# Kernel optimization log

Measured on AMD Instinct MI355X. Metric: run time of the kernel, lower is better.

Reference implementation:

```python
import jax, jax.numpy as jnp
import numpy as np

N, E = 10000, 100000
WIDTH, KER_WIDTH, DEPTH = 32, 128, 3
EDGE_ATTR_DIM, IN_WIDTH, OUT_WIDTH, COORD_DIM = 6, 3, 1, 3


def _glorot(k, fan_in, fan_out):
    return jax.random.normal(k, (fan_in, fan_out), jnp.float32) / np.sqrt(fan_in).astype(np.float32)


def setup_inputs() -> dict:
    key = jax.random.key(0)
    ks = jax.random.split(key, 16)
    z = lambda n: jnp.zeros((n,), jnp.float32)
    return {
        "x": jax.random.normal(ks[0], (N, IN_WIDTH), jnp.float32),
        "edge_index": jax.random.randint(ks[1], (2, E), 0, N),
        "edge_attr": jax.random.normal(ks[2], (E, EDGE_ATTR_DIM), jnp.float32),
        "coords_init": jax.random.normal(ks[3], (N, COORD_DIM), jnp.float32),
        "fc1_w": _glorot(ks[4], IN_WIDTH, WIDTH), "fc1_b": z(WIDTH),
        "ker_w1": _glorot(ks[5], EDGE_ATTR_DIM + 1, KER_WIDTH // 2), "ker_b1": z(KER_WIDTH // 2),
        "ker_w2": _glorot(ks[6], KER_WIDTH // 2, KER_WIDTH), "ker_b2": z(KER_WIDTH),
        "ker_w3": _glorot(ks[7], KER_WIDTH, WIDTH * WIDTH), "ker_b3": z(WIDTH * WIDTH),
        "cm_w1": _glorot(ks[8], WIDTH, WIDTH), "cm_b1": z(WIDTH),
        "cm_w2": _glorot(ks[9], WIDTH, 1) * 1e-3,  # xavier gain=0.001 coord head, no bias
        "fc2_w1": _glorot(ks[10], WIDTH, 2 * WIDTH), "fc2_b1": z(2 * WIDTH),
        "fc2_w2": _glorot(ks[11], 2 * WIDTH, OUT_WIDTH), "fc2_b2": z(OUT_WIDTH),
    }


def _seg_mean(data, seg, n):
    s = jax.ops.segment_sum(data, seg, num_segments=n)
    c = jax.ops.segment_sum(jnp.ones((seg.shape[0], 1), data.dtype), seg, num_segments=n)
    return s / jnp.clip(c, 1.0)


def reference(x, edge_index, edge_attr, coords_init,
              fc1_w, fc1_b, ker_w1, ker_b1, ker_w2, ker_b2, ker_w3, ker_b3,
              cm_w1, cm_b1, cm_w2, fc2_w1, fc2_b1, fc2_w2, fc2_b2):
    row, col = edge_index[0], edge_index[1]
    h = x @ fc1_w + fc1_b                                   # [N, W]
    coord = coords_init
    for _ in range(DEPTH):
        coord_diff = coord[row] - coord[col]                # [E, 3]
        radial = jnp.sum(coord_diff * coord_diff, axis=-1, keepdims=True)
        kin = jnp.concatenate([edge_attr, radial], axis=-1)  # [E, ker_in]
        k = jax.nn.relu(kin @ ker_w1 + ker_b1)
        k = jax.nn.relu(k @ ker_w2 + ker_b2)
        Wk = (k @ ker_w3 + ker_b3).reshape(E, WIDTH, WIDTH)  # per-edge kernel matrix
        m = jnp.einsum('eij,ej->ei', Wk, h[col])             # per-edge message [E, W]
        phi = jax.nn.relu(m @ cm_w1 + cm_b1) @ cm_w2         # [E, 1]
        coord = coord + _seg_mean(coord_diff * phi, row, N)  # equivariant coord update
        h = jax.nn.relu(h + _seg_mean(m, row, N))            # GKN node update
    out = jax.nn.relu(h @ fc2_w1 + fc2_b1) @ fc2_w2 + fc2_b2  # [N, out_width]
    return out, coord
```

## Files before the change

### kernel.cpp

```cpp
#include <hip/hip_runtime.h>
#include <hip/hip_bf16.h>

#define NN 10000
#define NE 100000

typedef __bf16 bf16x8 __attribute__((ext_vector_type(8)));
typedef float  f32x4  __attribute__((ext_vector_type(4)));

__device__ __forceinline__ f32x4 relu4(f32x4 a) {
    a.x = fmaxf(a.x, 0.f); a.y = fmaxf(a.y, 0.f);
    a.z = fmaxf(a.z, 0.f); a.w = fmaxf(a.w, 0.f);
    return a;
}


__global__ void k_deg(const int* __restrict__ eidx, int* __restrict__ deg) {
    int e = blockIdx.x * blockDim.x + threadIdx.x;
    if (e < NE) atomicAdd(&deg[eidx[e]], 1);
}

__global__ void k_scan(const int* __restrict__ deg, int* __restrict__ rowptr,
                       int* __restrict__ cursor, float* __restrict__ deg_inv) {
    __shared__ int ssum[256];
    const int tid = threadIdx.x;
    const int CH = 40;
    const int base = tid * CH;
    int s = 0;
    for (int i = 0; i < CH; ++i) { int n = base + i; if (n < NN) s += deg[n]; }
    ssum[tid] = s;
    __syncthreads();
    for (int off = 1; off < 256; off <<= 1) {
        int t = (tid >= off) ? ssum[tid - off] : 0;
        __syncthreads();
        ssum[tid] += t;
        __syncthreads();
    }
    int run = ssum[tid] - s;
    for (int i = 0; i < CH; ++i) {
        int n = base + i;
        if (n < NN) {
            int d = deg[n];
            rowptr[n] = run; cursor[n] = run; run += d;
            deg_inv[n] = 1.0f / (float)(d > 1 ? d : 1);
        }
    }
    if (tid == 255) rowptr[NN] = ssum[255];
}

__global__ void k_fill(const int* __restrict__ eidx, int* __restrict__ cursor,
                       int* __restrict__ ebyrow, int* __restrict__ pos_r) {
    int e = blockIdx.x * blockDim.x + threadIdx.x;
    if (e < NE) {
        int r = eidx[e];
        int slot = atomicAdd(&cursor[r], 1);
        ebyrow[slot] = e;
        pos_r[e] = slot;
    }
}

__global__ void k_setup(const float* __restrict__ w3, __bf16* __restrict__ w3sw,
                        const float* __restrict__ w2, __bf16* __restrict__ w2sw,
                        const float* __restrict__ x, const float* __restrict__ fc1w,
                        const float* __restrict__ fc1b, const float* __restrict__ cinit,
                        float* __restrict__ h, float* __restrict__ coord) {
    int t = blockIdx.x * blockDim.x + threadIdx.x;
    if (t < 131072) {
        int jj = t & 7;
        int L  = (t >> 3) & 63;
        int ks = (t >> 9) & 3;
        int jt = (t >> 11) & 1;
        int i  = t >> 12;
        int c    = ks*32 + (L >> 4)*8 + jj;
        int colv = i*32 + jt*16 + (L & 15);
        w3sw[t] = (__bf16)w3[c*1024 + colv];
    } else if (t < 139264) {
        int u = t - 131072;
        int jj = u & 7;
        int L  = (u >> 3) & 63;
        int ks = (u >> 9) & 1;
        int nt = u >> 10;
        int c1 = ks*32 + (L >> 4)*8 + jj;
        int c2 = nt*16 + (L & 15);
        w2sw[u] = (__bf16)w2[c1*128 + c2];
    } else if (t < 139264 + NN) {
        int n = t - 139264;
        float x0 = x[n*3+0], x1 = x[n*3+1], x2 = x[n*3+2];
        #pragma unroll
        for (int j = 0; j < 32; j += 4) {
            f32x4 a = *(const f32x4*)(fc1b + j);
            a += x0 * (*(const f32x4*)(fc1w + 0*32 + j));
            a += x1 * (*(const f32x4*)(fc1w + 1*32 + j));
            a += x2 * (*(const f32x4*)(fc1w + 2*32 + j));
            *(f32x4*)(h + n*32 + j) = a;
        }
        coord[n*3+0] = cinit[n*3+0];
        coord[n*3+1] = cinit[n*3+1];
        coord[n*3+2] = cinit[n*3+2];
    }
}

__global__ __launch_bounds__(256, 2)
void k_layer(const float* __restrict__ coord, const int* __restrict__ eidx,
             const float* __restrict__ eattr,
             const float* __restrict__ w1, const float* __restrict__ b1,
             const __bf16* __restrict__ w2sw, const float* __restrict__ b2,
             const __bf16* __restrict__ w3sw, const float* __restrict__ b3,
             const float* __restrict__ h,
             const float* __restrict__ cm_w1, const float* __restrict__ cm_b1,
             const float* __restrict__ cm_w2, const int* __restrict__ pos_r,
             float* __restrict__ cds, float* __restrict__ m_s,
             float* __restrict__ phis) {
    __shared__ float smem[4 * 64 * 36];
    __bf16* kt1 = (__bf16*)smem;
    __bf16* kt2 = (__bf16*)smem + 4608;
    const int lane = threadIdx.x & 63;
    const int wave = threadIdx.x >> 6;
    const int q = lane >> 4, t = lane & 15;
    const int base = blockIdx.x * 64;

    const int eg = base + lane;
    const int egc = eg < NE ? eg : NE - 1;
    const bool wvalid = eg < NE;
    const int pos = pos_r[egc];

    int col = eidx[NE + egc];
    float hcol[32];
    {
        const f32x4* hp = (const f32x4*)(h + (size_t)col * 32);
        #pragma unroll
        for (int v = 0; v < 8; ++v) {
            f32x4 hv = hp[v];
            hcol[v*4+0] = hv.x; hcol[v*4+1] = hv.y; hcol[v*4+2] = hv.z; hcol[v*4+3] = hv.w;
        }
    }
    bf16x8 bcur[8];
    {
        const __bf16* wb0 = w3sw + (size_t)(wave * 8) * 4096;
        #pragma unroll
        for (int f = 0; f < 8; ++f)
            bcur[f] = *(const bf16x8*)(wb0 + (f*64 + lane) * 8);
    }

    {
        int r = eidx[egc];
        float dx = coord[r*3+0] - coord[col*3+0];
        float dy = coord[r*3+1] - coord[col*3+1];
        float dz = coord[r*3+2] - coord[col*3+2];
        float rad = dx*dx + dy*dy + dz*dz;
        if (wave == 0 && wvalid) {
            f32x4 cdv = {dx, dy, dz, rad};
            *(f32x4*)(cds + (size_t)pos*4) = cdv;
        }
        float kin[7];
        #pragma unroll
        for (int a = 0; a < 6; ++a) kin[a] = eattr[(size_t)egc*6 + a];
        kin[6] = rad;

        const int g0 = wave * 16;
        f32x4 acc1[4];
        #pragma unroll
        for (int g = 0; g < 4; ++g) acc1[g] = *(const f32x4*)(b1 + g0 + g*4);
        #pragma unroll
        for (int t7 = 0; t7 < 7; ++t7) {
            float kv = kin[t7];
            #pragma unroll
            for (int g = 0; g < 4; ++g)
                acc1[g] += kv * (*(const f32x4*)(w1 + t7*64 + g0 + g*4));
        }
        #pragma unroll
        for (int cc = 0; cc < 2; ++cc) {
            f32x4 a0 = relu4(acc1[cc*2]), a1 = relu4(acc1[cc*2+1]);
            bf16x8 pk = {(__bf16)a0.x, (__bf16)a0.y, (__bf16)a0.z, (__bf16)a0.w,
                         (__bf16)a1.x, (__bf16)a1.y, (__bf16)a1.z, (__bf16)a1.w};
            int chunk = wave*2 + cc;
            *(bf16x8*)(kt1 + lane*72 + ((chunk ^ (lane & 7)) * 8)) = pk;
        }
    }
    __syncthreads();

    {
        bf16x8 af[4][2];
        #pragma unroll
        for (int mt = 0; mt < 4; ++mt) {
            int ep = mt*16 + t;
            #pragma unroll
            for (int ks = 0; ks < 2; ++ks)
                af[mt][ks] = *(const bf16x8*)(kt1 + ep*72 + (((ks*4 + q) ^ (ep & 7)) * 8));
        }
        #pragma unroll
        for (int nn = 0; nn < 2; ++nn) {
            int nt = wave*2 + nn;
            f32x4 a2[4];
            #pragma unroll
            for (int mt = 0; mt < 4; ++mt) a2[mt] = (f32x4){0.f, 0.f, 0.f, 0.f};
            #pragma unroll
            for (int ks = 0; ks < 2; ++ks) {
                bf16x8 bf_ = *(const bf16x8*)(w2sw + ((nt*2 + ks)*64 + lane) * 8);
                #pragma unroll
                for (int mt = 0; mt < 4; ++mt)
                    a2[mt] = __builtin_amdgcn_mfma_f32_16x16x32_bf16(af[mt][ks], bf_, a2[mt], 0, 0, 0);
            }
            float bias = b2[nt*16 + t];
            int chunk = nt*2 + (t >> 3);
            int tin = t & 7;
            #pragma unroll
            for (int mt = 0; mt < 4; ++mt) {
                #pragma unroll
                for (int rr = 0; rr < 4; ++rr) {
                    int row = mt*16 + q*4 + rr;
                    kt2[row*128 + ((chunk ^ (row & 15)) * 8) + tin] =
                        (__bf16)fmaxf(a2[mt][rr] + bias, 0.f);
                }
            }
        }
    }
    __syncthreads();

    bf16x8 afrag[4][4];
    #pragma unroll
    for (int mt = 0; mt < 4; ++mt) {
        int ep = mt*16 + t;
        #pragma unroll
        for (int ks = 0; ks < 4; ++ks) {
            int ck = ks*4 + q;
            afrag[mt][ks] = *(const bf16x8*)(kt2 + ep*128 + ((ck ^ (ep & 15)) * 8));
        }
    }
    __syncthreads();

    float* wkw = smem + wave * (64 * 36);
    const float* wkrow = wkw + lane * 36;
    float mv[8];

    #pragma unroll
    for (int ii = 0; ii < 8; ++ii) {
        const int i = wave * 8 + ii;
        f32x4 acc[4][2];
        #pragma unroll
        for (int mt = 0; mt < 4; ++mt) {
            acc[mt][0] = (f32x4){0.f, 0.f, 0.f, 0.f};
            acc[mt][1] = (f32x4){0.f, 0.f, 0.f, 0.f};
        }
        #pragma unroll
        for (int jt = 0; jt < 2; ++jt) {
            #pragma unroll
            for (int ks = 0; ks < 4; ++ks) {
                bf16x8 bfrag = bcur[jt*4 + ks];
                #pragma unroll
                for (int mt = 0; mt < 4; ++mt)
                    acc[mt][jt] = __builtin_amdgcn_mfma_f32_16x16x32_bf16(
                        afrag[mt][ks], bfrag, acc[mt][jt], 0, 0, 0);
            }
        }
        if (ii < 7) {
            const __bf16* wbn = w3sw + (size_t)(i + 1) * 4096;
            #pragma unroll
            for (int f = 0; f < 8; ++f)
                bcur[f] = *(const bf16x8*)(wbn + (f*64 + lane) * 8);
        }
        float bias0 = b3[i*32 + t];
        float bias1 = b3[i*32 + 16 + t];
        #pragma unroll
        for (int mt = 0; mt < 4; ++mt) {
            #pragma unroll
            for (int r = 0; r < 4; ++r) {
                int row = mt*16 + q*4 + r;
                wkw[row*36 + t]      = acc[mt][0][r] + bias0;
                wkw[row*36 + 16 + t] = acc[mt][1][r] + bias1;
            }
        }
        float s = 0.f;
        #pragma unroll
        for (int v = 0; v < 8; ++v) {
            f32x4 wv = *(const f32x4*)(wkrow + v*4);
            s += wv.x*hcol[v*4+0] + wv.y*hcol[v*4+1] + wv.z*hcol[v*4+2] + wv.w*hcol[v*4+3];
        }
        mv[ii] = s;
    }

    if (wvalid) {
        f32x4 v0 = {mv[0], mv[1], mv[2], mv[3]};
        f32x4 v1 = {mv[4], mv[5], mv[6], mv[7]};
        *(f32x4*)(m_s + (size_t)pos*32 + wave*8)     = v0;
        *(f32x4*)(m_s + (size_t)pos*32 + wave*8 + 4) = v1;
    }

    __syncthreads();
    float* mvx = smem;
    #pragma unroll
    for (int ii = 0; ii < 8; ++ii)
        mvx[(wave*8 + ii)*65 + lane] = mv[ii];
    __syncthreads();
    if (wave == 0) {
        float m2[32];
        #pragma unroll
        for (int i = 0; i < 32; ++i) m2[i] = mvx[i*65 + lane];
        float phi = 0.f;
        for (int o = 0; o < 32; o += 4) {
            f32x4 a = *(const f32x4*)(cm_b1 + o);
            #pragma unroll
            for (int i = 0; i < 32; ++i)
                a += m2[i] * (*(const f32x4*)(cm_w1 + i*32 + o));
            a = relu4(a);
            f32x4 w2 = *(const f32x4*)(cm_w2 + o);
            phi += a.x*w2.x + a.y*w2.y + a.z*w2.z + a.w*w2.w;
        }
        if (wvalid) phis[pos] = phi;
    }
}

__global__ __launch_bounds__(256, 4)
void k_gather(const int* __restrict__ rowptr,
              const float* __restrict__ m_s, const float* __restrict__ phis,
              const float* __restrict__ cds, const float* __restrict__ deg_inv,
              float* __restrict__ coord, float* __restrict__ h,
              const float* __restrict__ fw1, const float* __restrict__ fb1,
              const float* __restrict__ fw2, const float* __restrict__ fb2,
              float* __restrict__ out, int dofinal) {
    int tid = blockIdx.x * blockDim.x + threadIdx.x;
    int n = tid >> 3, sub = tid & 7;
    if (n >= NN) return;
    int st = rowptr[n], en = rowptr[n+1];
    f32x4 am0 = {0.f, 0.f, 0.f, 0.f}, am1 = {0.f, 0.f, 0.f, 0.f};
    int p = st;
    for (; p + 1 < en; p += 2) {
        am0 += *(const f32x4*)(m_s + (size_t)p*32 + sub*4);
        am1 += *(const f32x4*)(m_s + (size_t)(p+1)*32 + sub*4);
    }
    if (p < en) am0 += *(const f32x4*)(m_s + (size_t)p*32 + sub*4);
    f32x4 am = am0 + am1;

    float di = deg_inv[n];
    f32x4 hv = *(const f32x4*)(h + (size_t)n*32 + sub*4);
    hv = relu4(hv + am * di);

    float c0 = 0.f, c1 = 0.f, c2 = 0.f;
    if (sub == 0) {
        float cx0 = 0.f, cy0 = 0.f, cz0 = 0.f;
        float cx1 = 0.f, cy1 = 0.f, cz1 = 0.f;
        int pp = st;
        for (; pp + 1 < en; pp += 2) {
            f32x4 cd0 = *(const f32x4*)(cds + (size_t)pp*4);
            f32x4 cd1 = *(const f32x4*)(cds + (size_t)(pp+1)*4);
            float p0 = phis[pp], p1 = phis[pp+1];
            cx0 += cd0.x * p0; cy0 += cd0.y * p0; cz0 += cd0.z * p0;
            cx1 += cd1.x * p1; cy1 += cd1.y * p1; cz1 += cd1.z * p1;
        }
        if (pp < en) {
            f32x4 cd0 = *(const f32x4*)(cds + (size_t)pp*4);
            float p0 = phis[pp];
            cx0 += cd0.x * p0; cy0 += cd0.y * p0; cz0 += cd0.z * p0;
        }
        c0 = coord[n*3+0] + (cx0 + cx1) * di;
        c1 = coord[n*3+1] + (cy0 + cy1) * di;
        c2 = coord[n*3+2] + (cz0 + cz1) * di;
    }

    if (!dofinal) {
        *(f32x4*)(h + (size_t)n*32 + sub*4) = hv;
        if (sub == 0) {
            coord[n*3+0] = c0; coord[n*3+1] = c1; coord[n*3+2] = c2;
        }
        return;
    }

    const int gbase = (tid & 63) & 56;
    float hreg[32];
    #pragma unroll
    for (int s2 = 0; s2 < 8; ++s2) {
        hreg[s2*4+0] = __shfl(hv.x, gbase + s2, 64);
        hreg[s2*4+1] = __shfl(hv.y, gbase + s2, 64);
        hreg[s2*4+2] = __shfl(hv.z, gbase + s2, 64);
        hreg[s2*4+3] = __shfl(hv.w, gbase + s2, 64);
    }
    float po = 0.f;
    #pragma unroll
    for (int oo = 0; oo < 8; oo += 4) {
        int o = sub*8 + oo;
        f32x4 a = *(const f32x4*)(fb1 + o);
        #pragma unroll
        for (int i = 0; i < 32; ++i)
            a += hreg[i] * (*(const f32x4*)(fw1 + i*64 + o));
        a = relu4(a);
        f32x4 w2 = *(const f32x4*)(fw2 + o);
        po += a.x*w2.x + a.y*w2.y + a.z*w2.z + a.w*w2.w;
    }
    po += __shfl_xor(po, 1, 64);
    po += __shfl_xor(po, 2, 64);
    po += __shfl_xor(po, 4, 64);
    if (sub == 0) {
        out[n] = po + fb2[0];
        out[NN + n*3 + 0] = c0;
        out[NN + n*3 + 1] = c1;
        out[NN + n*3 + 2] = c2;
    }
}


extern "C" void kernel_launch(void* const* d_in, const int* in_sizes, int n_in,
                              void* d_out, int out_size, void* d_ws, size_t ws_size,
                              hipStream_t stream) {
    const float* x      = (const float*)d_in[0];
    const int*   eidx   = (const int*)  d_in[1];
    const float* eattr  = (const float*)d_in[2];
    const float* cinit  = (const float*)d_in[3];
    const float* fc1w   = (const float*)d_in[4];
    const float* fc1b   = (const float*)d_in[5];
    const float* kw1    = (const float*)d_in[6];
    const float* kb1    = (const float*)d_in[7];
    const float* kw2    = (const float*)d_in[8];
    const float* kb2    = (const float*)d_in[9];
    const float* kw3    = (const float*)d_in[10];
    const float* kb3    = (const float*)d_in[11];
    const float* cmw1   = (const float*)d_in[12];
    const float* cmb1   = (const float*)d_in[13];
    const float* cmw2   = (const float*)d_in[14];
    const float* f2w1   = (const float*)d_in[15];
    const float* f2b1   = (const float*)d_in[16];
    const float* f2w2   = (const float*)d_in[17];
    const float* f2b2   = (const float*)d_in[18];
    float* out = (float*)d_out;

    char* p = (char*)d_ws;
    auto carve = [&](size_t bytes) {
        void* r = (void*)p;
        p += (bytes + 255) & ~(size_t)255;
        return r;
    };
    float*  h        = (float*) carve((size_t)NN * 32 * 4);
    float*  coord    = (float*) carve((size_t)NN * 3 * 4);
    int*    deg      = (int*)   carve((size_t)NN * 4);
    float*  deg_inv  = (float*) carve((size_t)NN * 4);
    int*    rowptr   = (int*)   carve((size_t)(NN + 1) * 4);
    int*    cursor   = (int*)   carve((size_t)NN * 4);
    int*    ebyrow   = (int*)   carve((size_t)NE * 4);
    int*    pos_r    = (int*)   carve((size_t)NE * 4);
    float*  cds      = (float*) carve((size_t)NE * 4 * 4);
    float*  m_s      = (float*) carve((size_t)NE * 32 * 4);
    float*  phis     = (float*) carve((size_t)NE * 4);
    __bf16* w3sw     = (__bf16*)carve((size_t)131072 * 2);
    __bf16* w2sw     = (__bf16*)carve((size_t)8192 * 2);

    const int TB = 256;
    dim3 gE((NE + TB - 1) / TB), b(TB);
    dim3 gS((139264 + NN + TB - 1) / TB);
    dim3 gG((NE + 63) / 64);
    dim3 gA((NN*8 + TB - 1) / TB);

    hipMemsetAsync(deg, 0, (size_t)NN * 4, stream);
    k_deg  <<<gE, b, 0, stream>>>(eidx, deg);
    k_scan <<<1, b, 0, stream>>>(deg, rowptr, cursor, deg_inv);
    k_fill <<<gE, b, 0, stream>>>(eidx, cursor, ebyrow, pos_r);
    k_setup<<<gS, b, 0, stream>>>(kw3, w3sw, kw2, w2sw, x, fc1w, fc1b, cinit, h, coord);

    for (int d = 0; d < 3; ++d) {
        k_layer<<<gG, b, 0, stream>>>(coord, eidx, eattr, kw1, kb1, w2sw, kb2,
                                      w3sw, kb3, h, cmw1, cmb1, cmw2, pos_r,
                                      cds, m_s, phis);
        k_gather<<<gA, b, 0, stream>>>(rowptr, m_s, phis, cds, deg_inv, coord, h,
                                       f2w1, f2b1, f2w2, f2b2, out, d == 2 ? 1 : 0);
    }
}
```

Measured before the change: 359.2 us.

## Store per-edge kernel matrix as packed bf16 in LDS, fuse degree count into setup

The per-edge 32x32 kernel matrix staged in shared memory is now stored as packed bf16 pairs with an XOR swizzle instead of padded fp32. This halves LDS footprint and traffic and removes a barrier, since the wave-private region no longer overlaps the shared kt buffers. The degree count is folded into the setup kernel, the scan uses 1024 threads, and the unused ebyrow array is dropped, which cuts launches. The Wk values are rounded to bf16 before the matvec with h, adding some precision loss.

Result: faster. 342.5 us (-4.6%).

```diff
diff --git a/kernel.cpp b/kernel.cpp
--- a/kernel.cpp
+++ b/kernel.cpp
@@ -6,6 +6,7 @@
 
 typedef __bf16 bf16x8 __attribute__((ext_vector_type(8)));
 typedef float  f32x4  __attribute__((ext_vector_type(4)));
+typedef unsigned int u32x4 __attribute__((ext_vector_type(4)));
 
 __device__ __forceinline__ f32x4 relu4(f32x4 a) {
     a.x = fmaxf(a.x, 0.f); a.y = fmaxf(a.y, 0.f);
@@ -14,55 +15,12 @@
 }
 
 
-__global__ void k_deg(const int* __restrict__ eidx, int* __restrict__ deg) {
-    int e = blockIdx.x * blockDim.x + threadIdx.x;
-    if (e < NE) atomicAdd(&deg[eidx[e]], 1);
-}
-
-__global__ void k_scan(const int* __restrict__ deg, int* __restrict__ rowptr,
-                       int* __restrict__ cursor, float* __restrict__ deg_inv) {
-    __shared__ int ssum[256];
-    const int tid = threadIdx.x;
-    const int CH = 40;
-    const int base = tid * CH;
-    int s = 0;
-    for (int i = 0; i < CH; ++i) { int n = base + i; if (n < NN) s += deg[n]; }
-    ssum[tid] = s;
-    __syncthreads();
-    for (int off = 1; off < 256; off <<= 1) {
-        int t = (tid >= off) ? ssum[tid - off] : 0;
-        __syncthreads();
-        ssum[tid] += t;
-        __syncthreads();
-    }
-    int run = ssum[tid] - s;
-    for (int i = 0; i < CH; ++i) {
-        int n = base + i;
-        if (n < NN) {
-            int d = deg[n];
-            rowptr[n] = run; cursor[n] = run; run += d;
-            deg_inv[n] = 1.0f / (float)(d > 1 ? d : 1);
-        }
-    }
-    if (tid == 255) rowptr[NN] = ssum[255];
-}
-
-__global__ void k_fill(const int* __restrict__ eidx, int* __restrict__ cursor,
-                       int* __restrict__ ebyrow, int* __restrict__ pos_r) {
-    int e = blockIdx.x * blockDim.x + threadIdx.x;
-    if (e < NE) {
-        int r = eidx[e];
-        int slot = atomicAdd(&cursor[r], 1);
-        ebyrow[slot] = e;
-        pos_r[e] = slot;
-    }
-}
-
 __global__ void k_setup(const float* __restrict__ w3, __bf16* __restrict__ w3sw,
                         const float* __restrict__ w2, __bf16* __restrict__ w2sw,
                         const float* __restrict__ x, const float* __restrict__ fc1w,
                         const float* __restrict__ fc1b, const float* __restrict__ cinit,
-                        float* __restrict__ h, float* __restrict__ coord) {
+                        float* __restrict__ h, float* __restrict__ coord,
+                        const int* __restrict__ eidx, int* __restrict__ deg) {
     int t = blockIdx.x * blockDim.x + threadIdx.x;
     if (t < 131072) {
         int jj = t & 7;
@@ -96,6 +54,47 @@
         coord[n*3+0] = cinit[n*3+0];
         coord[n*3+1] = cinit[n*3+1];
         coord[n*3+2] = cinit[n*3+2];
+    } else if (t < 139264 + NN + NE) {
+        int e = t - 139264 - NN;
+        atomicAdd(&deg[eidx[e]], 1);
+    }
+}
+
+__global__ __launch_bounds__(1024, 1)
+void k_scan(const int* __restrict__ deg, int* __restrict__ rowptr,
+            int* __restrict__ cursor, float* __restrict__ deg_inv) {
+    __shared__ int ssum[1024];
+    const int tid = threadIdx.x;
+    const int CH = 10;
+    const int base = tid * CH;
+    int s = 0;
+    for (int i = 0; i < CH; ++i) { int n = base + i; if (n < NN) s += deg[n]; }
+    ssum[tid] = s;
+    __syncthreads();
+    for (int off = 1; off < 1024; off <<= 1) {
+        int t = (tid >= off) ? ssum[tid - off] : 0;
+        __syncthreads();
+        ssum[tid] += t;
+        __syncthreads();
+    }
+    int run = ssum[tid] - s;
+    for (int i = 0; i < CH; ++i) {
+        int n = base + i;
+        if (n < NN) {
+            int d = deg[n];
+            rowptr[n] = run; cursor[n] = run; run += d;
+            deg_inv[n] = 1.0f / (float)(d > 1 ? d : 1);
+        }
+    }
+    if (tid == 1023) rowptr[NN] = ssum[1023];
+}
+
+__global__ void k_fill(const int* __restrict__ eidx, int* __restrict__ cursor,
+                       int* __restrict__ pos_r) {
+    int e = blockIdx.x * blockDim.x + threadIdx.x;
+    if (e < NE) {
+        int r = eidx[e];
+        pos_r[e] = atomicAdd(&cursor[r], 1);
     }
 }
 
@@ -110,9 +109,9 @@
              const float* __restrict__ cm_w2, const int* __restrict__ pos_r,
              float* __restrict__ cds, float* __restrict__ m_s,
              float* __restrict__ phis) {
-    __shared__ float smem[4 * 64 * 36];
-    __bf16* kt1 = (__bf16*)smem;
-    __bf16* kt2 = (__bf16*)smem + 4608;
+    __shared__ unsigned smem_u[9216];
+    __bf16* kt1 = (__bf16*)smem_u;
+    __bf16* kt2 = (__bf16*)smem_u + 10240;
     const int lane = threadIdx.x & 63;
     const int wave = threadIdx.x >> 6;
     const int q = lane >> 4, t = lane & 15;
@@ -226,10 +225,10 @@
             afrag[mt][ks] = *(const bf16x8*)(kt2 + ep*128 + ((ck ^ (ep & 15)) * 8));
         }
     }
-    __syncthreads();
-
-    float* wkw = smem + wave * (64 * 36);
-    const float* wkrow = wkw + lane * 36;
+
+    unsigned* wkw = smem_u + wave * 1280;
+    const unsigned* wkrow = wkw + lane * 20;
+    const int maskr = (lane ^ (lane >> 3)) & 3;
     float mv[8];
 
     #pragma unroll
@@ -265,15 +264,26 @@
             #pragma unroll
             for (int r = 0; r < 4; ++r) {
                 int row = mt*16 + q*4 + r;
-                wkw[row*36 + t]      = acc[mt][0][r] + bias0;
-                wkw[row*36 + 16 + t] = acc[mt][1][r] + bias1;
+                float a0 = acc[mt][0][r] + bias0;
+                float a1 = acc[mt][1][r] + bias1;
+                unsigned u0 = (unsigned)__builtin_bit_cast(unsigned short, (__bf16)a0);
+                unsigned u1 = (unsigned)__builtin_bit_cast(unsigned short, (__bf16)a1);
+                int msk = (row ^ (row >> 3)) & 3;
+                wkw[row*20 + ((((t >> 2) ^ msk) << 2) | (t & 3))] = u0 | (u1 << 16);
             }
         }
         float s = 0.f;
         #pragma unroll
-        for (int v = 0; v < 8; ++v) {
-            f32x4 wv = *(const f32x4*)(wkrow + v*4);
-            s += wv.x*hcol[v*4+0] + wv.y*hcol[v*4+1] + wv.z*hcol[v*4+2] + wv.w*hcol[v*4+3];
+        for (int j = 0; j < 4; ++j) {
+            u32x4 wv = *(const u32x4*)(wkrow + ((j ^ maskr) << 2));
+            #pragma unroll
+            for (int k = 0; k < 4; ++k) {
+                unsigned w = wv[k];
+                int c = j*4 + k;
+                float flo = __uint_as_float(w << 16);
+                float fhi = __uint_as_float(w & 0xFFFF0000u);
+                s += flo * hcol[c] + fhi * hcol[16 + c];
+            }
         }
         mv[ii] = s;
     }
@@ -286,7 +296,7 @@
     }
 
     __syncthreads();
-    float* mvx = smem;
+    float* mvx = (float*)smem_u;
     #pragma unroll
     for (int ii = 0; ii < 8; ++ii)
         mvx[(wave*8 + ii)*65 + lane] = mv[ii];
@@ -433,7 +443,6 @@
     float*  deg_inv  = (float*) carve((size_t)NN * 4);
     int*    rowptr   = (int*)   carve((size_t)(NN + 1) * 4);
     int*    cursor   = (int*)   carve((size_t)NN * 4);
-    int*    ebyrow   = (int*)   carve((size_t)NE * 4);
     int*    pos_r    = (int*)   carve((size_t)NE * 4);
     float*  cds      = (float*) carve((size_t)NE * 4 * 4);
     float*  m_s      = (float*) carve((size_t)NE * 32 * 4);
@@ -443,15 +452,15 @@
 
     const int TB = 256;
     dim3 gE((NE + TB - 1) / TB), b(TB);
-    dim3 gS((139264 + NN + TB - 1) / TB);
+    dim3 gS((139264 + NN + NE + TB - 1) / TB);
     dim3 gG((NE + 63) / 64);
     dim3 gA((NN*8 + TB - 1) / TB);
 
     hipMemsetAsync(deg, 0, (size_t)NN * 4, stream);
-    k_deg  <<<gE, b, 0, stream>>>(eidx, deg);
-    k_scan <<<1, b, 0, stream>>>(deg, rowptr, cursor, deg_inv);
-    k_fill <<<gE, b, 0, stream>>>(eidx, cursor, ebyrow, pos_r);
-    k_setup<<<gS, b, 0, stream>>>(kw3, w3sw, kw2, w2sw, x, fc1w, fc1b, cinit, h, coord);
+    k_setup<<<gS, b, 0, stream>>>(kw3, w3sw, kw2, w2sw, x, fc1w, fc1b, cinit,
+                                  h, coord, eidx, deg);
+    k_scan <<<1, dim3(1024), 0, stream>>>(deg, rowptr, cursor, deg_inv);
+    k_fill <<<gE, b, 0, stream>>>(eidx, cursor, pos_r);
 
     for (int d = 0; d < 3; ++d) {
         k_layer<<<gG, b, 0, stream>>>(coord, eidx, eattr, kw1, kb1, w2sw, kb2,
```
